# Kernel tuning notes

Measured on AMD Instinct MI355X. Metric: run time of the kernel, lower is better.

Reference implementation:

```python
import jax, jax.numpy as jnp
import numpy as np

N_NODES = 100000
N_EDGES = 1600000
IN_CH, HID_CH, OUT_CH = 128, 128, 64


def _spmm(row, col, val, x, n):
    # COO sparse @ dense: out[r] += val_e * x[col_e]
    gathered = val[:, None] * x[col]  # [E, d]
    return jax.ops.segment_sum(gathered, row, num_segments=n)


def setup_inputs() -> dict:
    key = jax.random.key(0)
    ks = jax.random.split(key, 8)
    x = jax.random.normal(ks[0], (N_NODES, IN_CH), dtype=jnp.float32)
    adj_row = jax.random.randint(ks[1], (N_EDGES,), 0, N_NODES)
    adj_col = jax.random.randint(ks[2], (N_EDGES,), 0, N_NODES)
    adj_val = jax.random.uniform(ks[3], (N_EDGES,), dtype=jnp.float32)
    w1 = jax.random.normal(ks[4], (IN_CH, HID_CH), dtype=jnp.float32) * (1.0 / np.sqrt(IN_CH))
    b1 = jax.random.normal(ks[5], (HID_CH,), dtype=jnp.float32) * 0.01
    w2 = jax.random.normal(ks[6], (HID_CH, OUT_CH), dtype=jnp.float32) * (1.0 / np.sqrt(HID_CH))
    b2 = jax.random.normal(ks[7], (OUT_CH,), dtype=jnp.float32) * 0.01
    return {"x": x, "adj_row": adj_row, "adj_col": adj_col, "adj_val": adj_val,
            "w1": w1, "b1": b1, "w2": w2, "b2": b2}


def reference(x, adj_row, adj_col, adj_val, w1, b1, w2, b2):
    n = x.shape[0]
    # layer 1: spmm -> linear -> relu
    h = _spmm(adj_row, adj_col, adj_val, x, n)
    h = jax.nn.relu(h @ w1 + b1)
    # layer 2: spmm -> linear
    h = _spmm(adj_row, adj_col, adj_val, h, n)
    return h @ w2 + b2
```

## Files before the change

### kernel.cpp

```cpp
#include <hip/hip_runtime.h>


typedef __bf16 v8bf __attribute__((ext_vector_type(8)));
typedef float  v4f  __attribute__((ext_vector_type(4)));

#define MAXB 800

__device__ __forceinline__ unsigned short f2bf(float f) {
    unsigned u = __float_as_uint(f);
    unsigned r = u + 0x7fffu + ((u >> 16) & 1u);
    return (unsigned short)(r >> 16);
}

__global__ __launch_bounds__(256) void hist_prep(const int* __restrict__ arow,
                                                 int* __restrict__ counts, int E, int B,
                                                 const float* __restrict__ w1,
                                                 const float* __restrict__ w2,
                                                 unsigned short* __restrict__ w1T,
                                                 unsigned short* __restrict__ w2T,
                                                 int* __restrict__ rowptr,
                                                 int2* __restrict__ epkS, int N) {
    const int tid = threadIdx.x;
    int gi = blockIdx.x * 256 + tid;
    if (gi < 16384) {
        int n = gi >> 7, k = gi & 127;
        w1T[gi] = f2bf(w1[k * 128 + n]);
    } else if (gi < 24576) {
        int i2 = gi - 16384;
        int n = i2 >> 7, k = i2 & 127;
        w2T[i2] = f2bf(w2[k * 64 + n]);
    } else if (gi < 24576 + 32) {
        epkS[E + (gi - 24576)] = make_int2(0, 0);
    } else if (gi == 24576 + 32) {
        rowptr[N] = E;
    }
    __shared__ int lh[MAXB];
    for (int i = tid; i < B; i += 256) lh[i] = 0;
    __syncthreads();
    const int base = blockIdx.x * 4096;
#pragma unroll
    for (int j = 0; j < 16; ++j) {
        int i = base + j * 256 + tid;
        if (i < E) atomicAdd(&lh[arow[i] >> 7], 1);
    }
    __syncthreads();
    for (int i = tid; i < B; i += 256) {
        int c = lh[i];
        if (c) atomicAdd(&counts[i], c);
    }
}

__global__ __launch_bounds__(256) void scan_s(const int* __restrict__ counts,
                                              int* __restrict__ boff,
                                              int* __restrict__ gcursor, int B, int E) {
    __shared__ int lds[256];
    const int t = threadIdx.x;
    const int b0 = t * 4;
    int v[4];
    int s = 0;
#pragma unroll
    for (int j = 0; j < 4; ++j) {
        v[j] = (b0 + j < B) ? counts[b0 + j] : 0;
        s += v[j];
    }
    lds[t] = s;
    __syncthreads();
    for (int off = 1; off < 256; off <<= 1) {
        int tmp = 0;
        if (t >= off) tmp = lds[t - off];
        __syncthreads();
        if (t >= off) lds[t] += tmp;
        __syncthreads();
    }
    int run = (t > 0) ? lds[t - 1] : 0;
#pragma unroll
    for (int j = 0; j < 4; ++j) {
        if (b0 + j < B) {
            boff[b0 + j] = run;
            gcursor[b0 + j] = run;
        }
        run += v[j];
    }
    if (t == 255) boff[B] = E;
}

__global__ __launch_bounds__(256) void partition_k(const int* __restrict__ arow,
                                                   const int* __restrict__ acol,
                                                   const float* __restrict__ aval,
                                                   int* __restrict__ gcursor,
                                                   int2* __restrict__ epk, int E, int B) {
    __shared__ int2 ldata[4096];
    __shared__ int ldest[4096];
    __shared__ int lhist[MAXB];
    __shared__ int lscan[MAXB];
    __shared__ int ldelta[MAXB];
    __shared__ int lcur[MAXB];
    __shared__ int stmp[256];
    const int tid = threadIdx.x;
    const int base = blockIdx.x * 4096;
    const int cnt = min(4096, E - base);

    for (int i = tid; i < MAXB; i += 256) {
        lhist[i] = 0;
        lcur[i] = 0;
    }
    __syncthreads();

    int rr[16];
#pragma unroll
    for (int j = 0; j < 16; ++j) {
        int i = base + j * 256 + tid;
        rr[j] = (i < E) ? arow[i] : -1;
        if (rr[j] >= 0) atomicAdd(&lhist[rr[j] >> 7], 1);
    }
    __syncthreads();

    const int b0 = tid * 4;
    int v[4];
    int s = 0;
#pragma unroll
    for (int j = 0; j < 4; ++j) {
        v[j] = (b0 + j < MAXB) ? lhist[b0 + j] : 0;
        s += v[j];
    }
    stmp[tid] = s;
    __syncthreads();
    for (int off = 1; off < 256; off <<= 1) {
        int tmp = 0;
        if (tid >= off) tmp = stmp[tid - off];
        __syncthreads();
        if (tid >= off) stmp[tid] += tmp;
        __syncthreads();
    }
    int run = (tid > 0) ? stmp[tid - 1] : 0;
#pragma unroll
    for (int j = 0; j < 4; ++j) {
        if (b0 + j < MAXB) lscan[b0 + j] = run;
        run += v[j];
    }
    __syncthreads();

    for (int b = tid; b < B; b += 256) {
        int c = lhist[b];
        if (c) ldelta[b] = atomicAdd(&gcursor[b], c) - lscan[b];
    }
    __syncthreads();

#pragma unroll
    for (int j = 0; j < 16; ++j) {
        int i = base + j * 256 + tid;
        if (i < E) {
            int r = rr[j];
            int b = r >> 7;
            int lp = atomicAdd(&lcur[b], 1);
            int slot = lscan[b] + lp;
            int pk = acol[i] | ((r & 127) << 17);
            ldata[slot] = make_int2(pk, __float_as_int(aval[i]));
            ldest[slot] = ldelta[b] + slot;
        }
    }
    __syncthreads();

    for (int s2 = tid; s2 < cnt; s2 += 256) epk[ldest[s2]] = ldata[s2];
}

template <int NC, bool AF32>
__device__ __forceinline__ void gemm_body(const void* __restrict__ A,
                                          const unsigned short* __restrict__ wT,
                                          unsigned short* __restrict__ y, int M,
                                          int bid, char* smem) {
    constexpr int KP = 136;
    constexpr int NT = NC / 16;
    unsigned short* wl = (unsigned short*)smem;
    const int tid = threadIdx.x;
    for (int idx = tid; idx < NC * 16; idx += 256) {
        int n = idx >> 4, kc = idx & 15;
        *(uint4*)&wl[n * KP + kc * 8] = *(const uint4*)&wT[n * 128 + kc * 8];
    }
    __syncthreads();

    const int wave = tid >> 6;
    const int lane = tid & 63;
    const int m = lane & 15;
    const int q = lane >> 4;
    const int rowbase = bid * 64 + wave * 16;
    const int rowc = min(rowbase + m, M - 1);

    v4f acc[NT] = {};
    union LU { uint4 qv; v8bf b; };

#pragma unroll
    for (int ks = 0; ks < 4; ++ks) {
        const int k0 = ks * 32 + q * 8;
        v8bf a;
        if (AF32) {
            const float* Ap = (const float*)A + (size_t)rowc * 128 + k0;
            float4 f0 = *(const float4*)Ap;
            float4 f1 = *(const float4*)(Ap + 4);
            union { unsigned short s[8]; v8bf b; } cv;
            cv.s[0] = f2bf(f0.x); cv.s[1] = f2bf(f0.y);
            cv.s[2] = f2bf(f0.z); cv.s[3] = f2bf(f0.w);
            cv.s[4] = f2bf(f1.x); cv.s[5] = f2bf(f1.y);
            cv.s[6] = f2bf(f1.z); cv.s[7] = f2bf(f1.w);
            a = cv.b;
        } else {
            LU lu;
            lu.qv = *(const uint4*)((const unsigned short*)A + (size_t)rowc * 128 + k0);
            a = lu.b;
        }
#pragma unroll
        for (int nt = 0; nt < NT; ++nt) {
            v8bf b = *(const v8bf*)&wl[(nt * 16 + m) * KP + k0];
            acc[nt] = __builtin_amdgcn_mfma_f32_16x16x32_bf16(a, b, acc[nt], 0, 0, 0);
        }
    }
#pragma unroll
    for (int nt = 0; nt < NT; ++nt) {
#pragma unroll
        for (int r = 0; r < 4; ++r) {
            int orow = rowbase + q * 4 + r;
            if (orow < M) y[(size_t)orow * NC + nt * 16 + m] = f2bf(acc[nt][r]);
        }
    }
}

__global__ __launch_bounds__(256) void sort_gemm1(const int* __restrict__ boff,
                                                  const int2* __restrict__ epk,
                                                  int2* __restrict__ epkS,
                                                  int* __restrict__ rowptr, int N, int B,
                                                  const float* __restrict__ x,
                                                  const unsigned short* __restrict__ w1T,
                                                  unsigned short* __restrict__ y1b) {
    __shared__ __align__(16) char smem[34816];
    const int tid = threadIdx.x;
    if (blockIdx.x >= B) {
        gemm_body<128, true>(x, w1T, y1b, N, blockIdx.x - B, smem);
        return;
    }
    int2* sorted = (int2*)smem;
    int*  sc     = (int*)(smem + 32768);
    int*  lcur   = (int*)(smem + 32768 + 512);
    const int b = blockIdx.x;
    const int s = boff[b], e = boff[b + 1];
    const int cnt = min(e - s, 4096);
    if (tid < 128) sc[tid] = 0;
    __syncthreads();
    for (int i = s + tid; i < e; i += 256) {
        int rl = (epk[i].x >> 17) & 127;
        atomicAdd(&sc[rl], 1);
    }
    __syncthreads();
    int hv = (tid < 128) ? sc[tid] : 0;
    for (int off = 1; off < 128; off <<= 1) {
        int add = 0;
        if (tid < 128 && tid >= off) add = sc[tid - off];
        __syncthreads();
        if (tid < 128 && tid >= off) sc[tid] += add;
        __syncthreads();
    }
    if (tid < 128) {
        int ex = sc[tid] - hv;
        lcur[tid] = ex;
        int r = b * 128 + tid;
        if (r < N) rowptr[r] = s + ex;
    }
    __syncthreads();
    for (int i = s + tid; i < e; i += 256) {
        int2 p = epk[i];
        int rl = (p.x >> 17) & 127;
        int slot = atomicAdd(&lcur[rl], 1);
        if (slot < 4096) sorted[slot] = make_int2(p.x & 0x1FFFF, p.y);
    }
    __syncthreads();
    for (int i = tid; i < cnt; i += 256) epkS[s + i] = sorted[i];
}

__global__ __launch_bounds__(256) void spmm_gemm2(const int* __restrict__ rowptr,
                                                  const int2* __restrict__ ep,
                                                  const unsigned short* __restrict__ y1b,
                                                  const float* __restrict__ b1,
                                                  const unsigned short* __restrict__ w2T,
                                                  unsigned short* __restrict__ y2b, int N) {
    constexpr int KP = 136;
    __shared__ unsigned short h1[64 * KP];
    const int tid = threadIdx.x;
    const int wave = tid >> 6, lane = tid & 63;
    const int eslot = lane >> 4;
    const int cb = lane & 15;
    const int rowbase = blockIdx.x * 64;
    const unsigned* y32 = (const unsigned*)y1b;
    const float4 bb0 = *(const float4*)&b1[8 * cb];
    const float4 bb1 = *(const float4*)&b1[8 * cb + 4];

    const int r0 = rowbase + wave * 16;
    int e_prev = (r0 < N) ? __builtin_amdgcn_readfirstlane(rowptr[r0]) : 0;
    for (int i = 0; i < 16; ++i) {
        const int r = r0 + i;
        float a[8] = {0.f, 0.f, 0.f, 0.f, 0.f, 0.f, 0.f, 0.f};
        if (r < N) {
            const int s = e_prev;
            const int e = __builtin_amdgcn_readfirstlane(rowptr[r + 1]);
            e_prev = e;
            int2 cur[4];
#pragma unroll
            for (int k = 0; k < 4; ++k) cur[k] = ep[s + 4 * k + eslot];
            for (int j = s; j < e; j += 16) {
                int2 nxt[4];
#pragma unroll
                for (int k = 0; k < 4; ++k) nxt[k] = ep[j + 16 + 4 * k + eslot];
                uint4 g[4];
                float v[4];
#pragma unroll
                for (int k = 0; k < 4; ++k) {
                    v[k] = (j + 4 * k + eslot < e) ? __int_as_float(cur[k].y) : 0.f;
                    if (j + 4 * k < e)
                        g[k] = *(const uint4*)(y32 + (((unsigned)cur[k].x) << 6) + (cb << 2));
                    else
                        g[k] = make_uint4(0u, 0u, 0u, 0u);
                }
#pragma unroll
                for (int k = 0; k < 4; ++k) {
                    a[0] += v[k] * __uint_as_float(g[k].x << 16);
                    a[1] += v[k] * __uint_as_float(g[k].x & 0xffff0000u);
                    a[2] += v[k] * __uint_as_float(g[k].y << 16);
                    a[3] += v[k] * __uint_as_float(g[k].y & 0xffff0000u);
                    a[4] += v[k] * __uint_as_float(g[k].z << 16);
                    a[5] += v[k] * __uint_as_float(g[k].z & 0xffff0000u);
                    a[6] += v[k] * __uint_as_float(g[k].w << 16);
                    a[7] += v[k] * __uint_as_float(g[k].w & 0xffff0000u);
                }
#pragma unroll
                for (int k = 0; k < 4; ++k) cur[k] = nxt[k];
            }
        }
#pragma unroll
        for (int t = 0; t < 8; ++t) a[t] += __shfl_xor(a[t], 16);
#pragma unroll
        for (int t = 0; t < 8; ++t) a[t] += __shfl_xor(a[t], 32);
        if (lane < 16) {
            float f0 = fmaxf(a[0] + bb0.x, 0.f);
            float f1 = fmaxf(a[1] + bb0.y, 0.f);
            float f2 = fmaxf(a[2] + bb0.z, 0.f);
            float f3 = fmaxf(a[3] + bb0.w, 0.f);
            float f4 = fmaxf(a[4] + bb1.x, 0.f);
            float f5 = fmaxf(a[5] + bb1.y, 0.f);
            float f6 = fmaxf(a[6] + bb1.z, 0.f);
            float f7 = fmaxf(a[7] + bb1.w, 0.f);
            uint4 pk;
            pk.x = ((unsigned)f2bf(f1) << 16) | f2bf(f0);
            pk.y = ((unsigned)f2bf(f3) << 16) | f2bf(f2);
            pk.z = ((unsigned)f2bf(f5) << 16) | f2bf(f4);
            pk.w = ((unsigned)f2bf(f7) << 16) | f2bf(f6);
            *(uint4*)&h1[(wave * 16 + i) * KP + 8 * cb] = pk;
        }
    }
    __syncthreads();

    const int m = lane & 15, q = lane >> 4;
    v4f acc[4] = {};
#pragma unroll
    for (int ks = 0; ks < 4; ++ks) {
        const int k0 = ks * 32 + q * 8;
        v8bf av = *(const v8bf*)&h1[(wave * 16 + m) * KP + k0];
#pragma unroll
        for (int nt = 0; nt < 4; ++nt) {
            v8bf b = *(const v8bf*)&w2T[(nt * 16 + m) * 128 + k0];
            acc[nt] = __builtin_amdgcn_mfma_f32_16x16x32_bf16(av, b, acc[nt], 0, 0, 0);
        }
    }
#pragma unroll
    for (int nt = 0; nt < 4; ++nt) {
#pragma unroll
        for (int r = 0; r < 4; ++r) {
            int orow = rowbase + wave * 16 + q * 4 + r;
            if (orow < N) y2b[(size_t)orow * 64 + nt * 16 + m] = f2bf(acc[nt][r]);
        }
    }
}

__global__ __launch_bounds__(256) void spmm64(const int* __restrict__ rowptr,
                                              const int2* __restrict__ ep,
                                              const unsigned short* __restrict__ yb,
                                              const float* __restrict__ bias,
                                              float* __restrict__ outp, int N) {
    const int row = (blockIdx.x * 256 + threadIdx.x) >> 6;
    const int lane = threadIdx.x & 63;
    if (row >= N) return;
    const int eslot = lane >> 3;
    const int cb = lane & 7;
    const unsigned* y32 = (const unsigned*)yb;
    const int s = __builtin_amdgcn_readfirstlane(rowptr[row]);
    const int e = __builtin_amdgcn_readfirstlane(rowptr[row + 1]);
    float a[8] = {0.f, 0.f, 0.f, 0.f, 0.f, 0.f, 0.f, 0.f};
    int2 cur[2];
#pragma unroll
    for (int k = 0; k < 2; ++k) cur[k] = ep[s + 8 * k + eslot];
    for (int j = s; j < e; j += 16) {
        int2 nxt[2];
#pragma unroll
        for (int k = 0; k < 2; ++k) nxt[k] = ep[j + 16 + 8 * k + eslot];
        uint4 g[2];
        float v[2];
#pragma unroll
        for (int k = 0; k < 2; ++k) {
            v[k] = (j + 8 * k + eslot < e) ? __int_as_float(cur[k].y) : 0.f;
            if (j + 8 * k < e)
                g[k] = *(const uint4*)(y32 + (((unsigned)cur[k].x) << 5) + (cb << 2));
            else
                g[k] = make_uint4(0u, 0u, 0u, 0u);
        }
#pragma unroll
        for (int k = 0; k < 2; ++k) {
            a[0] += v[k] * __uint_as_float(g[k].x << 16);
            a[1] += v[k] * __uint_as_float(g[k].x & 0xffff0000u);
            a[2] += v[k] * __uint_as_float(g[k].y << 16);
            a[3] += v[k] * __uint_as_float(g[k].y & 0xffff0000u);
            a[4] += v[k] * __uint_as_float(g[k].z << 16);
            a[5] += v[k] * __uint_as_float(g[k].z & 0xffff0000u);
            a[6] += v[k] * __uint_as_float(g[k].w << 16);
            a[7] += v[k] * __uint_as_float(g[k].w & 0xffff0000u);
        }
#pragma unroll
        for (int k = 0; k < 2; ++k) cur[k] = nxt[k];
    }
#pragma unroll
    for (int t = 0; t < 8; ++t) a[t] += __shfl_xor(a[t], 8);
#pragma unroll
    for (int t = 0; t < 8; ++t) a[t] += __shfl_xor(a[t], 16);
#pragma unroll
    for (int t = 0; t < 8; ++t) a[t] += __shfl_xor(a[t], 32);
    if (lane < 8) {
        const float4 c0 = *(const float4*)&bias[8 * cb];
        const float4 c1 = *(const float4*)&bias[8 * cb + 4];
        float4 o0 = make_float4(a[0] + c0.x, a[1] + c0.y, a[2] + c0.z, a[3] + c0.w);
        float4 o1 = make_float4(a[4] + c1.x, a[5] + c1.y, a[6] + c1.z, a[7] + c1.w);
        float* op = outp + (size_t)row * 64 + 8 * cb;
        *(float4*)op = o0;
        *(float4*)(op + 4) = o1;
    }
}

extern "C" void kernel_launch(void* const* d_in, const int* in_sizes, int n_in,
                              void* d_out, int out_size, void* d_ws, size_t ws_size,
                              hipStream_t stream) {
    const float* x    = (const float*)d_in[0];
    const int*   arow = (const int*)d_in[1];
    const int*   acol = (const int*)d_in[2];
    const float* aval = (const float*)d_in[3];
    const float* w1   = (const float*)d_in[4];
    const float* b1   = (const float*)d_in[5];
    const float* w2   = (const float*)d_in[6];
    const float* b2   = (const float*)d_in[7];
    float*       out  = (float*)d_out;

    const int N = in_sizes[0] / 128;
    const int E = in_sizes[1];
    const int B = (N + 127) >> 7;

    char* p = (char*)d_ws;
    auto alloc = [&](size_t bytes) {
        char* r = p;
        p += (bytes + 255) & ~(size_t)255;
        return r;
    };
    int*            counts  = (int*)alloc((size_t)MAXB * 4);
    int*            boff    = (int*)alloc((size_t)(MAXB + 1) * 4);
    int*            gcursor = (int*)alloc((size_t)MAXB * 4);
    int*            rowptr  = (int*)alloc((size_t)(N + 1) * 4);
    int2*           epkS    = (int2*)alloc((size_t)(E + 32) * 8);
    unsigned short* w1T     = (unsigned short*)alloc(128 * 128 * 2);
    unsigned short* w2T     = (unsigned short*)alloc(64 * 128 * 2);
    unsigned short* y1b     = (unsigned short*)alloc((size_t)N * 128 * 2);
    int2*           epk     = (int2*)alloc((size_t)E * 8);
    unsigned short* y2b     = (unsigned short*)alloc((size_t)N * 64 * 2);

    const int gemm_blocks = (N + 63) / 64;
    const int pb = (E + 4095) / 4096;

    hipMemsetAsync(counts, 0, (size_t)MAXB * 4, stream);
    hist_prep<<<pb, 256, 0, stream>>>(arow, counts, E, B, w1, w2, w1T, w2T,
                                      rowptr, epkS, N);
    scan_s<<<1, 256, 0, stream>>>(counts, boff, gcursor, B, E);
    partition_k<<<pb, 256, 0, stream>>>(arow, acol, aval, gcursor, epk, E, B);
    sort_gemm1<<<B + gemm_blocks, 256, 0, stream>>>(boff, epk, epkS, rowptr, N, B,
                                                    x, w1T, y1b);
    spmm_gemm2<<<gemm_blocks, 256, 0, stream>>>(rowptr, epkS, y1b, b1, w2T, y2b, N);
    const int spmm_blocks = (N + 3) / 4;
    spmm64<<<spmm_blocks, 256, 0, stream>>>(rowptr, epkS, y2b, b2, out, N);
}
```

Before: 290.9 us.

## Software-pipeline row gathers across rows in fused spmm_gemm2 kernel

```diff
diff --git a/kernel.cpp b/kernel.cpp
--- a/kernel.cpp
+++ b/kernel.cpp
@@ -293,44 +293,90 @@
     const float4 bb1 = *(const float4*)&b1[8 * cb + 4];
 
     const int r0 = rowbase + wave * 16;
-    int e_prev = (r0 < N) ? __builtin_amdgcn_readfirstlane(rowptr[r0]) : 0;
+    const int rp = rowptr[min(r0 + min((int)lane, 17), N)];
+#define BND(i) __shfl(rp, (i))
+
+    int2 epc[8], epn[8];
+    uint4 gcv[8];
+    {
+        const int s0 = BND(0), e0 = BND(1);
+#pragma unroll
+        for (int u = 0; u < 8; ++u) epc[u] = ep[s0 + 4 * u + eslot];
+        const int s1 = BND(1);
+#pragma unroll
+        for (int u = 0; u < 8; ++u) epn[u] = ep[s1 + 4 * u + eslot];
+#pragma unroll
+        for (int u = 0; u < 8; ++u) {
+            gcv[u] = make_uint4(0u, 0u, 0u, 0u);
+            if (s0 + 4 * u < e0)
+                gcv[u] = *(const uint4*)(y32 + (((unsigned)epc[u].x) << 6) + (cb << 2));
+        }
+    }
+
+#pragma unroll 1
     for (int i = 0; i < 16; ++i) {
-        const int r = r0 + i;
+        const int si = BND(i), ei = BND(i + 1);
+        int2 epn2[8];
+        if (i < 14) {
+            const int s2 = BND(i + 2);
+#pragma unroll
+            for (int u = 0; u < 8; ++u) epn2[u] = ep[s2 + 4 * u + eslot];
+        }
+        uint4 gn[8];
+        if (i < 15) {
+            const int sn = BND(i + 1), en = BND(i + 2);
+#pragma unroll
+            for (int u = 0; u < 8; ++u) {
+                gn[u] = make_uint4(0u, 0u, 0u, 0u);
+                if (sn + 4 * u < en)
+                    gn[u] = *(const uint4*)(y32 + (((unsigned)epn[u].x) << 6) + (cb << 2));
+            }
+        }
         float a[8] = {0.f, 0.f, 0.f, 0.f, 0.f, 0.f, 0.f, 0.f};
-        if (r < N) {
-            const int s = e_prev;
-            const int e = __builtin_amdgcn_readfirstlane(rowptr[r + 1]);
-            e_prev = e;
-            int2 cur[4];
-#pragma unroll
-            for (int k = 0; k < 4; ++k) cur[k] = ep[s + 4 * k + eslot];
-            for (int j = s; j < e; j += 16) {
-                int2 nxt[4];
-#pragma unroll
-                for (int k = 0; k < 4; ++k) nxt[k] = ep[j + 16 + 4 * k + eslot];
-                uint4 g[4];
-                float v[4];
-#pragma unroll
-                for (int k = 0; k < 4; ++k) {
-                    v[k] = (j + 4 * k + eslot < e) ? __int_as_float(cur[k].y) : 0.f;
-                    if (j + 4 * k < e)
-                        g[k] = *(const uint4*)(y32 + (((unsigned)cur[k].x) << 6) + (cb << 2));
-                    else
-                        g[k] = make_uint4(0u, 0u, 0u, 0u);
-                }
-#pragma unroll
-                for (int k = 0; k < 4; ++k) {
-                    a[0] += v[k] * __uint_as_float(g[k].x << 16);
-                    a[1] += v[k] * __uint_as_float(g[k].x & 0xffff0000u);
-                    a[2] += v[k] * __uint_as_float(g[k].y << 16);
-                    a[3] += v[k] * __uint_as_float(g[k].y & 0xffff0000u);
-                    a[4] += v[k] * __uint_as_float(g[k].z << 16);
-                    a[5] += v[k] * __uint_as_float(g[k].z & 0xffff0000u);
-                    a[6] += v[k] * __uint_as_float(g[k].w << 16);
-                    a[7] += v[k] * __uint_as_float(g[k].w & 0xffff0000u);
-                }
-#pragma unroll
-                for (int k = 0; k < 4; ++k) cur[k] = nxt[k];
+#pragma unroll
+        for (int u = 0; u < 4; ++u) {
+            const float v = (si + 4 * u + eslot < ei) ? __int_as_float(epc[u].y) : 0.f;
+            a[0] += v * __uint_as_float(gcv[u].x << 16);
+            a[1] += v * __uint_as_float(gcv[u].x & 0xffff0000u);
+            a[2] += v * __uint_as_float(gcv[u].y << 16);
+            a[3] += v * __uint_as_float(gcv[u].y & 0xffff0000u);
+            a[4] += v * __uint_as_float(gcv[u].z << 16);
+            a[5] += v * __uint_as_float(gcv[u].z & 0xffff0000u);
+            a[6] += v * __uint_as_float(gcv[u].w << 16);
+            a[7] += v * __uint_as_float(gcv[u].w & 0xffff0000u);
+        }
+        if (si + 16 < ei) {
+#pragma unroll
+            for (int u = 4; u < 8; ++u) {
+                const float v = (si + 4 * u + eslot < ei) ? __int_as_float(epc[u].y) : 0.f;
+                a[0] += v * __uint_as_float(gcv[u].x << 16);
+                a[1] += v * __uint_as_float(gcv[u].x & 0xffff0000u);
+                a[2] += v * __uint_as_float(gcv[u].y << 16);
+                a[3] += v * __uint_as_float(gcv[u].y & 0xffff0000u);
+                a[4] += v * __uint_as_float(gcv[u].z << 16);
+                a[5] += v * __uint_as_float(gcv[u].z & 0xffff0000u);
+                a[6] += v * __uint_as_float(gcv[u].w << 16);
+                a[7] += v * __uint_as_float(gcv[u].w & 0xffff0000u);
+            }
+        }
+        for (int j = si + 32; j < ei; j += 16) {
+            int2 ec2[4];
+#pragma unroll
+            for (int k = 0; k < 4; ++k) ec2[k] = ep[j + 4 * k + eslot];
+#pragma unroll
+            for (int k = 0; k < 4; ++k) {
+                uint4 g = make_uint4(0u, 0u, 0u, 0u);
+                if (j + 4 * k < ei)
+                    g = *(const uint4*)(y32 + (((unsigned)ec2[k].x) << 6) + (cb << 2));
+                const float v = (j + 4 * k + eslot < ei) ? __int_as_float(ec2[k].y) : 0.f;
+                a[0] += v * __uint_as_float(g.x << 16);
+                a[1] += v * __uint_as_float(g.x & 0xffff0000u);
+                a[2] += v * __uint_as_float(g.y << 16);
+                a[3] += v * __uint_as_float(g.y & 0xffff0000u);
+                a[4] += v * __uint_as_float(g.z << 16);
+                a[5] += v * __uint_as_float(g.z & 0xffff0000u);
+                a[6] += v * __uint_as_float(g.w << 16);
+                a[7] += v * __uint_as_float(g.w & 0xffff0000u);
             }
         }
 #pragma unroll
@@ -353,7 +399,19 @@
             pk.w = ((unsigned)f2bf(f7) << 16) | f2bf(f6);
             *(uint4*)&h1[(wave * 16 + i) * KP + 8 * cb] = pk;
         }
-    }
+        if (i < 15) {
+#pragma unroll
+            for (int u = 0; u < 8; ++u) {
+                epc[u] = epn[u];
+                gcv[u] = gn[u];
+            }
+        }
+        if (i < 14) {
+#pragma unroll
+            for (int u = 0; u < 8; ++u) epn[u] = epn2[u];
+        }
+    }
+#undef BND
     __syncthreads();
 
     const int m = lane & 15, q = lane >> 4;
```

Measured after the change: 303.3 us. 4.3% more time.

## Recast first-layer SpMM as MFMA over edge-chunk selection matrices

Applied to the files above, without the earlier changes.

```diff
diff --git a/kernel.cpp b/kernel.cpp
--- a/kernel.cpp
+++ b/kernel.cpp
@@ -3,6 +3,10 @@
 
 typedef __bf16 v8bf __attribute__((ext_vector_type(8)));
 typedef float  v4f  __attribute__((ext_vector_type(4)));
+typedef unsigned v2u __attribute__((ext_vector_type(2)));
+
+#define AS1 __attribute__((address_space(1)))
+#define AS3 __attribute__((address_space(3)))
 
 #define MAXB 800
 
@@ -10,6 +14,16 @@
     unsigned u = __float_as_uint(f);
     unsigned r = u + 0x7fffu + ((u >> 16) & 1u);
     return (unsigned short)(r >> 16);
+}
+
+__device__ __forceinline__ unsigned ldsaddr(const void* p) {
+    return (unsigned)(unsigned long long)(const AS3 char*)p;
+}
+
+__device__ __forceinline__ v2u tr16(unsigned a) {
+    v2u d;
+    asm volatile("ds_read_b64_tr_b16 %0, %1" : "=v"(d) : "v"(a));
+    return d;
 }
 
 __global__ __launch_bounds__(256) void hist_prep(const int* __restrict__ arow,
@@ -269,7 +283,7 @@
         int2 p = epk[i];
         int rl = (p.x >> 17) & 127;
         int slot = atomicAdd(&lcur[rl], 1);
-        if (slot < 4096) sorted[slot] = make_int2(p.x & 0x1FFFF, p.y);
+        if (slot < 4096) sorted[slot] = p;
     }
     __syncthreads();
     for (int i = tid; i < cnt; i += 256) epkS[s + i] = sorted[i];
@@ -282,82 +296,81 @@
                                                   const unsigned short* __restrict__ w2T,
                                                   unsigned short* __restrict__ y2b, int N) {
     constexpr int KP = 136;
-    __shared__ unsigned short h1[64 * KP];
+    __shared__ __align__(1024) char smem[40960];
     const int tid = threadIdx.x;
     const int wave = tid >> 6, lane = tid & 63;
-    const int eslot = lane >> 4;
-    const int cb = lane & 15;
+    char* NTc = smem + wave * 10240;
+    char* AT0 = NTc + 8192;
+    char* AT1 = NTc + 9216;
     const int rowbase = blockIdx.x * 64;
-    const unsigned* y32 = (const unsigned*)y1b;
-    const float4 bb0 = *(const float4*)&b1[8 * cb];
-    const float4 bb1 = *(const float4*)&b1[8 * cb + 4];
-
     const int r0 = rowbase + wave * 16;
-    int e_prev = (r0 < N) ? __builtin_amdgcn_readfirstlane(rowptr[r0]) : 0;
-    for (int i = 0; i < 16; ++i) {
-        const int r = r0 + i;
-        float a[8] = {0.f, 0.f, 0.f, 0.f, 0.f, 0.f, 0.f, 0.f};
-        if (r < N) {
-            const int s = e_prev;
-            const int e = __builtin_amdgcn_readfirstlane(rowptr[r + 1]);
-            e_prev = e;
-            int2 cur[4];
-#pragma unroll
-            for (int k = 0; k < 4; ++k) cur[k] = ep[s + 4 * k + eslot];
-            for (int j = s; j < e; j += 16) {
-                int2 nxt[4];
-#pragma unroll
-                for (int k = 0; k < 4; ++k) nxt[k] = ep[j + 16 + 4 * k + eslot];
-                uint4 g[4];
-                float v[4];
-#pragma unroll
-                for (int k = 0; k < 4; ++k) {
-                    v[k] = (j + 4 * k + eslot < e) ? __int_as_float(cur[k].y) : 0.f;
-                    if (j + 4 * k < e)
-                        g[k] = *(const uint4*)(y32 + (((unsigned)cur[k].x) << 6) + (cb << 2));
-                    else
-                        g[k] = make_uint4(0u, 0u, 0u, 0u);
-                }
-#pragma unroll
-                for (int k = 0; k < 4; ++k) {
-                    a[0] += v[k] * __uint_as_float(g[k].x << 16);
-                    a[1] += v[k] * __uint_as_float(g[k].x & 0xffff0000u);
-                    a[2] += v[k] * __uint_as_float(g[k].y << 16);
-                    a[3] += v[k] * __uint_as_float(g[k].y & 0xffff0000u);
-                    a[4] += v[k] * __uint_as_float(g[k].z << 16);
-                    a[5] += v[k] * __uint_as_float(g[k].z & 0xffff0000u);
-                    a[6] += v[k] * __uint_as_float(g[k].w << 16);
-                    a[7] += v[k] * __uint_as_float(g[k].w & 0xffff0000u);
-                }
-#pragma unroll
-                for (int k = 0; k < 4; ++k) cur[k] = nxt[k];
-            }
-        }
-#pragma unroll
-        for (int t = 0; t < 8; ++t) a[t] += __shfl_xor(a[t], 16);
-#pragma unroll
-        for (int t = 0; t < 8; ++t) a[t] += __shfl_xor(a[t], 32);
-        if (lane < 16) {
-            float f0 = fmaxf(a[0] + bb0.x, 0.f);
-            float f1 = fmaxf(a[1] + bb0.y, 0.f);
-            float f2 = fmaxf(a[2] + bb0.z, 0.f);
-            float f3 = fmaxf(a[3] + bb0.w, 0.f);
-            float f4 = fmaxf(a[4] + bb1.x, 0.f);
-            float f5 = fmaxf(a[5] + bb1.y, 0.f);
-            float f6 = fmaxf(a[6] + bb1.z, 0.f);
-            float f7 = fmaxf(a[7] + bb1.w, 0.f);
-            uint4 pk;
-            pk.x = ((unsigned)f2bf(f1) << 16) | f2bf(f0);
-            pk.y = ((unsigned)f2bf(f3) << 16) | f2bf(f2);
-            pk.z = ((unsigned)f2bf(f5) << 16) | f2bf(f4);
-            pk.w = ((unsigned)f2bf(f7) << 16) | f2bf(f6);
-            *(uint4*)&h1[(wave * 16 + i) * KP + 8 * cb] = pk;
-        }
-    }
-    __syncthreads();
-
+    const int si = __builtin_amdgcn_readfirstlane(rowptr[min(r0, N)]);
+    const int ei = __builtin_amdgcn_readfirstlane(rowptr[min(r0 + 16, N)]);
     const int m = lane & 15, q = lane >> 4;
-    v4f acc[4] = {};
+
+    float b1v[8];
+#pragma unroll
+    for (int h = 0; h < 8; ++h) b1v[h] = b1[h * 16 + m];
+
+    const unsigned trB = ldsaddr(NTc) + (unsigned)(q * 256 + m * 8);
+
+    v4f acc[8] = {};
+
+    for (int cb = si; cb < ei; cb += 32) {
+        const int2 pe = ep[cb + (lane & 31)];
+        const int colg = __shfl(pe.x & 0x1FFFF, lane >> 1);
+        const char* gp = (const char*)y1b + ((size_t)(unsigned)colg << 8) + ((lane & 1) << 4);
+#pragma unroll
+        for (int t = 0; t < 8; ++t)
+            __builtin_amdgcn_global_load_lds((const AS1 unsigned*)(gp + t * 32),
+                                             (AS3 unsigned*)(NTc + t * 1024),
+                                             16, 0, 0);
+        const uint4 z4 = make_uint4(0u, 0u, 0u, 0u);
+        *(uint4*)(AT0 + lane * 16) = z4;
+        *(uint4*)(AT1 + lane * 16) = z4;
+        if (lane < 32 && cb + lane < ei) {
+            const float v = __int_as_float(pe.y);
+            const unsigned short vh = f2bf(v);
+            const float vhf = __uint_as_float((unsigned)vh << 16);
+            const unsigned short vl = f2bf(v - vhf);
+            const int rl4 = (pe.x >> 17) & 15;
+            *(unsigned short*)(AT0 + rl4 * 64 + lane * 2) = vh;
+            *(unsigned short*)(AT1 + rl4 * 64 + lane * 2) = vl;
+        }
+        asm volatile("s_waitcnt vmcnt(0)" ::: "memory");
+        __builtin_amdgcn_sched_barrier(0);
+        v2u tr0[8], tr1[8];
+#pragma unroll
+        for (int h = 0; h < 8; ++h) {
+            tr0[h] = tr16(trB + h * 1024);
+            tr1[h] = tr16(trB + h * 1024 + 128);
+        }
+        const v8bf avh = *(const v8bf*)(AT0 + m * 64 + q * 16);
+        const v8bf avl = *(const v8bf*)(AT1 + m * 64 + q * 16);
+        asm volatile("s_waitcnt lgkmcnt(0)" ::: "memory");
+        __builtin_amdgcn_sched_barrier(0);
+#pragma unroll
+        for (int h = 0; h < 8; ++h) {
+            union { unsigned u[4]; v8bf b; } bu;
+            bu.u[0] = tr0[h][0]; bu.u[1] = tr0[h][1];
+            bu.u[2] = tr1[h][0]; bu.u[3] = tr1[h][1];
+            acc[h] = __builtin_amdgcn_mfma_f32_16x16x32_bf16(avh, bu.b, acc[h], 0, 0, 0);
+            acc[h] = __builtin_amdgcn_mfma_f32_16x16x32_bf16(avl, bu.b, acc[h], 0, 0, 0);
+        }
+    }
+    __syncthreads();
+    unsigned short* h1 = (unsigned short*)smem;
+#pragma unroll
+    for (int h = 0; h < 8; ++h) {
+#pragma unroll
+        for (int r = 0; r < 4; ++r) {
+            const float f = fmaxf(acc[h][r] + b1v[h], 0.f);
+            h1[(wave * 16 + q * 4 + r) * KP + h * 16 + m] = f2bf(f);
+        }
+    }
+    __syncthreads();
+
+    v4f acc2[4] = {};
 #pragma unroll
     for (int ks = 0; ks < 4; ++ks) {
         const int k0 = ks * 32 + q * 8;
@@ -365,7 +378,7 @@
 #pragma unroll
         for (int nt = 0; nt < 4; ++nt) {
             v8bf b = *(const v8bf*)&w2T[(nt * 16 + m) * 128 + k0];
-            acc[nt] = __builtin_amdgcn_mfma_f32_16x16x32_bf16(av, b, acc[nt], 0, 0, 0);
+            acc2[nt] = __builtin_amdgcn_mfma_f32_16x16x32_bf16(av, b, acc2[nt], 0, 0, 0);
         }
     }
 #pragma unroll
@@ -373,7 +386,7 @@
 #pragma unroll
         for (int r = 0; r < 4; ++r) {
             int orow = rowbase + wave * 16 + q * 4 + r;
-            if (orow < N) y2b[(size_t)orow * 64 + nt * 16 + m] = f2bf(acc[nt][r]);
+            if (orow < N) y2b[(size_t)orow * 64 + nt * 16 + m] = f2bf(acc2[nt][r]);
         }
     }
 }
@@ -405,7 +418,7 @@
         for (int k = 0; k < 2; ++k) {
             v[k] = (j + 8 * k + eslot < e) ? __int_as_float(cur[k].y) : 0.f;
             if (j + 8 * k < e)
-                g[k] = *(const uint4*)(y32 + (((unsigned)cur[k].x) << 5) + (cb << 2));
+                g[k] = *(const uint4*)(y32 + (((unsigned)(cur[k].x & 0x1FFFF)) << 5) + (cb << 2));
             else
                 g[k] = make_uint4(0u, 0u, 0u, 0u);
         }
```

Result: faster. 280.9 us (-3.4%).
